# Optimization experiments

Hardware: AMD Instinct MI355X
Metric: run time of the kernel (lower is better)

## Reference

```python
import jax, jax.numpy as jnp
import numpy as np

B, K, N, M = 32, 128, 128, 256  # batch, num_classes(==n_dim), n_dim, samples-per-matrix
EPSILON = 0.1
LAMBDA_SOFTMAX = 0.1
LEARNING_RATE = 0.01
BN_EPS = 1e-5


def setup_inputs() -> dict:
    key = jax.random.key(0)
    k1, k2, k3 = jax.random.split(key, 3)
    x = jax.random.normal(k1, (B, N, M), dtype=jnp.float32)
    A = jax.random.normal(k2, (K, N, N), dtype=jnp.float32) * 0.1
    EC_proto = jnp.einsum('kij,klj->kil', A, A)  # per-class PSD prototype covariances (K,N,N)
    EC_count = jax.random.uniform(k3, (K,), dtype=jnp.float32, minval=1.0, maxval=100.0)
    return {"x": x, "EC_proto": EC_proto, "EC_count": EC_count}


def reference(x, EC_proto, EC_count):
    n = x.shape[1]
    dtype = x.dtype
    # BatchNorm1d(num_classes, affine=False, track_running_stats=False): batch stats over (N, L)
    mean = x.mean(axis=(0, 2), keepdims=True)
    var = x.var(axis=(0, 2), keepdims=True)  # biased variance, as torch uses for normalization
    x = (x - mean) / jnp.sqrt(var + BN_EPS)

    eye = jnp.eye(n, dtype=dtype)
    total = EC_count.sum()
    has_counts = total > 1e-6

    # E branch: global expansion operator
    e_alpha = jnp.where(has_counts, n / (EPSILON * EPSILON * total), jnp.zeros((), dtype))
    e = e_alpha * jnp.linalg.inv(e_alpha * EC_proto.sum(0) + eye)  # (N,N)
    e_x_z = jnp.einsum('ij,bjm->bim', e, x)  # (B,N,M)

    # C branch: per-class compression operators
    bool_depth = (EC_count != 0).astype(dtype)  # (K,)
    count_fix = EC_count + (1.0 - bool_depth)
    c_alpha = (n / (count_fix * EPSILON * EPSILON) * bool_depth)[:, None, None]  # (K,1,1)
    c = c_alpha * jnp.linalg.inv(c_alpha * EC_proto + eye[None])  # (K,N,N)
    c_x_z = jnp.einsum('kij,bjm->bkim', c, x)  # (B,K,N,M)

    # Frobenius norm per (b,k), rescaled to sum to 10 over classes
    norm = jnp.sqrt((c_x_z * c_x_z).sum(axis=(2, 3)))  # (B,K)
    norm = 10.0 * norm / norm.sum(axis=1, keepdims=True)

    pi = jax.nn.softmax(-LAMBDA_SOFTMAX * norm, axis=1) * bool_depth  # (B,K)
    gama = jnp.where(has_counts, EC_count / total, jnp.zeros_like(EC_count))  # (K,)

    z_d = e_x_z - jnp.einsum('k,bkim,bk->bim', gama, c_x_z, pi)  # (B,N,M)
    return x + LEARNING_RATE * z_d
```

## Files before the change

kernel.cpp:

```cpp
#include <hip/hip_runtime.h>
#include <math.h>

#define Bb 32
#define Kk 128
#define Nn 128
#define Mm 256
#define EPS2 0.01f
#define LAMBDA_S 0.1f
#define LR 0.01f
#define BN_EPS_C 1e-5f

#define SWZ(c) (((c) & 14) | (((c) & 1) << 4) | (((c) >> 4) & 1))

__device__ __forceinline__ float readlane_f(float v, int lane) {
  return __int_as_float(__builtin_amdgcn_readlane(__float_as_int(v), lane));
}

__global__ void kA_bn_psum(const float* __restrict__ x, const float* __restrict__ P,
                           float* __restrict__ xn, float* __restrict__ Psum) {
  int t = threadIdx.x;
  if (blockIdx.x < 128) {
    int n = blockIdx.x;
    float v[32];
    float s = 0.f, s2 = 0.f;
    #pragma unroll
    for (int b = 0; b < Bb; ++b) {
      v[b] = x[(size_t)b * (Nn * Mm) + n * Mm + t];
      s += v[b];
      s2 += v[b] * v[b];
    }
    #pragma unroll
    for (int o = 32; o > 0; o >>= 1) {
      s += __shfl_down(s, o, 64);
      s2 += __shfl_down(s2, o, 64);
    }
    __shared__ float rs[4], rs2[4];
    if ((t & 63) == 0) { rs[t >> 6] = s; rs2[t >> 6] = s2; }
    __syncthreads();
    float S = rs[0] + rs[1] + rs[2] + rs[3];
    float S2 = rs2[0] + rs2[1] + rs2[2] + rs2[3];
    float mean = S * (1.0f / (Bb * Mm));
    float var = S2 * (1.0f / (Bb * Mm)) - mean * mean;
    float rstd = 1.0f / sqrtf(var + BN_EPS_C);
    #pragma unroll
    for (int b = 0; b < Bb; ++b)
      xn[(size_t)b * (Nn * Mm) + n * Mm + t] = (v[b] - mean) * rstd;
  } else {
    int e = (blockIdx.x - 128) * 256 + t;
    float s = 0.f;
    #pragma unroll 8
    for (int k = 0; k < Kk; ++k) s += P[(size_t)k * 16384 + e];
    Psum[e] = s;
  }
}

__global__ __launch_bounds__(512, 1) void k3S(
    const float* __restrict__ P, const float* __restrict__ Psum,
    const float* __restrict__ cnt, float* __restrict__ C,
    const float* __restrict__ xn, float* __restrict__ S) {
  __shared__ __align__(16) float LB[8448];
  int bx = blockIdx.x;
  int t = threadIdx.x;

  if (bx < 129) {
    float* Mt = LB;
    float* Rb = LB + 2112;
    float* redc = LB + 4160;
    int mat = bx;
    int tx = t & 15;
    int wy = t >> 4;

    float cv = cnt[t & 127];
    float sr = cv;
    #pragma unroll
    for (int o = 32; o > 0; o >>= 1) sr += __shfl_down(sr, o, 64);
    if ((t & 63) == 0) redc[t >> 6] = sr;
    __syncthreads();
    float total = redc[0] + redc[1];
    bool has = total > 1e-6f;
    float av;
    if (mat < 128) {
      float c = cnt[mat];
      float bk = (c != 0.0f) ? 1.0f : 0.0f;
      float cfix = c + (1.0f - bk);
      av = (float)Nn / (cfix * EPS2) * bk;
    } else {
      av = has ? ((float)Nn / (EPS2 * total)) : 0.0f;
    }
    const float* src = (mat < 128) ? (P + (size_t)mat * 16384) : Psum;

    float a[4][8];
    #pragma unroll
    for (int i = 0; i < 4; ++i) {
      int row = wy * 4 + i;
      float4 p0 = *(const float4*)&src[row * 128 + tx * 8];
      float4 p1 = *(const float4*)&src[row * 128 + tx * 8 + 4];
      a[i][0] = av * p0.x; a[i][1] = av * p0.y; a[i][2] = av * p0.z; a[i][3] = av * p0.w;
      a[i][4] = av * p1.x; a[i][5] = av * p1.y; a[i][6] = av * p1.z; a[i][7] = av * p1.w;
      if (tx == (wy >> 1)) a[i][(wy & 1) * 4 + i] += 1.0f;
    }

    for (int kb = 0; kb < 8; ++kb) {
      int k0 = kb * 16;
      if ((wy >> 2) == kb) {
        int d = wy & 3;
        #pragma unroll
        for (int i = 0; i < 4; ++i) {
          *(float4*)&Rb[(d * 4 + i) * 128 + SWZ(2 * tx) * 4] =
              make_float4(a[i][0], a[i][1], a[i][2], a[i][3]);
          *(float4*)&Rb[(d * 4 + i) * 128 + SWZ(2 * tx + 1) * 4] =
              make_float4(a[i][4], a[i][5], a[i][6], a[i][7]);
        }
      }
      if ((tx >> 1) == kb) {
        int dh = tx & 1;
        #pragma unroll
        for (int i = 0; i < 4; ++i)
          #pragma unroll
          for (int j = 0; j < 8; ++j)
            Mt[(dh * 8 + j) * 132 + wy * 4 + i] = a[i][j];
      }
      __syncthreads();

      if (t < 64) {
        int l = t;
        float m[2][16];
        #pragma unroll
        for (int d = 0; d < 2; ++d)
          #pragma unroll
          for (int j = 0; j < 16; ++j)
            m[d][j] = Mt[j * 132 + 2 * l + d];
        #pragma unroll
        for (int q = 0; q < 16; ++q) {
          int lq = (k0 + q) >> 1;
          float pr[16];
          #pragma unroll
          for (int j = 0; j < 16; ++j) pr[j] = readlane_f(m[q & 1][j], lq);
          float piv = pr[q];
          float r0 = __builtin_amdgcn_rcpf(piv);
          float pinv = r0 * (2.0f - piv * r0);
          #pragma unroll
          for (int d = 0; d < 2; ++d) {
            float f = m[d][q];
            bool isp = (2 * l + d == k0 + q);
            float g = isp ? (1.0f - pinv) : f * pinv;
            #pragma unroll
            for (int j = 0; j < 16; ++j) m[d][j] = fmaf(-g, pr[j], m[d][j]);
            m[d][q] = isp ? pinv : -g;
          }
        }
        #pragma unroll
        for (int d = 0; d < 2; ++d)
          #pragma unroll
          for (int j = 0; j < 16; ++j)
            Mt[j * 132 + 2 * l + d] = m[d][j];
      }
      __syncthreads();

      if ((wy >> 2) == kb) {
        #pragma unroll
        for (int i = 0; i < 4; ++i)
          #pragma unroll
          for (int j = 0; j < 8; ++j) a[i][j] = 0.0f;
      }
      #pragma unroll
      for (int q = 0; q < 16; ++q) {
        float4 m0 = *(const float4*)&Mt[q * 132 + wy * 4];
        float4 r0 = *(const float4*)&Rb[q * 128 + SWZ(2 * tx) * 4];
        float4 r1 = *(const float4*)&Rb[q * 128 + SWZ(2 * tx + 1) * 4];
        float mq[4] = {m0.x, m0.y, m0.z, m0.w};
        float rq[8] = {r0.x, r0.y, r0.z, r0.w, r1.x, r1.y, r1.z, r1.w};
        #pragma unroll
        for (int i = 0; i < 4; ++i)
          #pragma unroll
          for (int j = 0; j < 8; ++j)
            a[i][j] = fmaf(mq[i], rq[j], a[i][j]);
      }
      if ((tx >> 1) == kb) {
        int dh = tx & 1;
        #pragma unroll
        for (int j = 0; j < 8; ++j) {
          float4 v0 = *(const float4*)&Mt[(dh * 8 + j) * 132 + wy * 4];
          a[0][j] = v0.x; a[1][j] = v0.y; a[2][j] = v0.z; a[3][j] = v0.w;
        }
      }
      __syncthreads();
    }

    float* dst = C + (size_t)mat * 16384;
    #pragma unroll
    for (int i = 0; i < 4; ++i) {
      int row = wy * 4 + i;
      float4 v0 = make_float4(av * a[i][0], av * a[i][1], av * a[i][2], av * a[i][3]);
      float4 v1 = make_float4(av * a[i][4], av * a[i][5], av * a[i][6], av * a[i][7]);
      *(float4*)&dst[row * 128 + tx * 8] = v0;
      *(float4*)&dst[row * 128 + tx * 8 + 4] = v1;
    }
  } else {
    int bxx = bx - 129;
    int b = bxx >> 1;
    int jbase = (bxx & 1) * 64;
    float* X = LB;
    int tx = t & 15, wy = t >> 4;
    float acc[4][4] = {};
    for (int mc = 0; mc < Mm; mc += 64) {
      __syncthreads();
      #pragma unroll
      for (int c = 0; c < 16; ++c) {
        int e = c * 512 + t;
        int i = e >> 6, mm = e & 63;
        X[i * 65 + mm] = xn[(size_t)b * (Nn * Mm) + i * Mm + mc + mm];
      }
      __syncthreads();
      for (int mm = 0; mm < 64; ++mm) {
        float ai[4], bj[4];
        #pragma unroll
        for (int q = 0; q < 4; ++q) ai[q] = X[(wy * 4 + q) * 65 + mm];
        #pragma unroll
        for (int q = 0; q < 4; ++q) bj[q] = X[(jbase + tx * 4 + q) * 65 + mm];
        #pragma unroll
        for (int qi = 0; qi < 4; ++qi)
          #pragma unroll
          for (int qj = 0; qj < 4; ++qj)
            acc[qi][qj] = fmaf(ai[qi], bj[qj], acc[qi][qj]);
      }
    }
    float* dst = S + (size_t)b * 16384;
    #pragma unroll
    for (int qi = 0; qi < 4; ++qi) {
      float4 v = make_float4(acc[qi][0], acc[qi][1], acc[qi][2], acc[qi][3]);
      *(float4*)&dst[(wy * 4 + qi) * 128 + jbase + tx * 4] = v;
    }
  }
}

__global__ __launch_bounds__(256, 1) void kGN(const float* __restrict__ C,
                                              const float* __restrict__ S,
                                              float* __restrict__ norm2h) {
  __shared__ __align__(16) float LB[128 * 128];
  __shared__ float redb[4][32];
  int k = blockIdx.x >> 2, qh = blockIdx.x & 3;
  int t = threadIdx.x;
  const float* src = C + (size_t)k * 16384;
  for (int c = 0; c < 64; ++c) LB[c * 256 + t] = src[c * 256 + t];
  __syncthreads();
  int tx = t & 15, ty = t >> 4;
  int i0 = ty * 8, j0 = qh * 32 + tx * 2;
  float acc[8][2] = {};
  #pragma unroll 2
  for (int l = 0; l < 128; ++l) {
    float ai[8];
    *(float4*)&ai[0] = *(const float4*)&LB[l * 128 + i0];
    *(float4*)&ai[4] = *(const float4*)&LB[l * 128 + i0 + 4];
    float2 bj = *(const float2*)&LB[l * 128 + j0];
    #pragma unroll
    for (int qi = 0; qi < 8; ++qi) {
      acc[qi][0] = fmaf(ai[qi], bj.x, acc[qi][0]);
      acc[qi][1] = fmaf(ai[qi], bj.y, acc[qi][1]);
    }
  }
  __syncthreads();
  #pragma unroll
  for (int qi = 0; qi < 8; ++qi)
    *(float2*)&LB[(i0 + qi) * 32 + tx * 2] = make_float2(acc[qi][0], acc[qi][1]);
  __syncthreads();
  float nacc[32];
  #pragma unroll
  for (int b = 0; b < 32; ++b) nacc[b] = 0.0f;
  #pragma unroll
  for (int q = 0; q < 4; ++q) {
    int el = (q * 256 + t) * 4;
    float4 g = *(const float4*)&LB[el];
    int i = el >> 5, jl = el & 31;
    const float* sb = S + i * 128 + qh * 32 + jl;
    #pragma unroll
    for (int b = 0; b < 32; ++b) {
      float4 sv = *(const float4*)&sb[(size_t)b * 16384];
      nacc[b] = fmaf(g.x, sv.x, nacc[b]);
      nacc[b] = fmaf(g.y, sv.y, nacc[b]);
      nacc[b] = fmaf(g.z, sv.z, nacc[b]);
      nacc[b] = fmaf(g.w, sv.w, nacc[b]);
    }
  }
  #pragma unroll
  for (int b = 0; b < 32; ++b) {
    float v = nacc[b];
    #pragma unroll
    for (int o = 32; o > 0; o >>= 1) v += __shfl_down(v, o, 64);
    nacc[b] = v;
  }
  if ((t & 63) == 0) {
    int w = t >> 6;
    #pragma unroll
    for (int b = 0; b < 32; ++b) redb[w][b] = nacc[b];
  }
  __syncthreads();
  if (t < 32)
    norm2h[(size_t)k * 128 + qh * 32 + t] =
        redb[0][t] + redb[1][t] + redb[2][t] + redb[3][t];
}

__global__ void k7n(const float* __restrict__ norm2h, const float* __restrict__ cnt,
                    float* __restrict__ wT) {
  int b = blockIdx.x;
  int k = threadIdx.x;
  const float* nh = norm2h + (size_t)k * 128 + b;
  float n2 = nh[0] + nh[32] + nh[64] + nh[96];
  float norm = sqrtf(fmaxf(n2, 0.0f));
  float cv = cnt[k];
  __shared__ float r1[2], r2[2], r3[2];
  float tt = cv, r = norm;
  #pragma unroll
  for (int o = 32; o > 0; o >>= 1) {
    tt += __shfl_down(tt, o, 64);
    r += __shfl_down(r, o, 64);
  }
  if ((k & 63) == 0) { r1[k >> 6] = tt; r2[k >> 6] = r; }
  __syncthreads();
  float total = r1[0] + r1[1];
  float sumn = r2[0] + r2[1];
  float nr = 10.0f * norm / fmaxf(sumn, 1e-30f);
  float ex = expf(-LAMBDA_S * nr);
  float e2 = ex;
  #pragma unroll
  for (int o = 32; o > 0; o >>= 1) e2 += __shfl_down(e2, o, 64);
  if ((k & 63) == 0) r3[k >> 6] = e2;
  __syncthreads();
  float sume = r3[0] + r3[1];
  float bk = (cv != 0.0f) ? 1.0f : 0.0f;
  float pi = (ex / sume) * bk;
  float gama = (total > 1e-6f) ? (cv / total) : 0.0f;
  wT[k * 32 + b] = gama * pi;
}

__global__ __launch_bounds__(256, 1) void k8_k(const float* __restrict__ C,
                                               const float* __restrict__ E,
                                               const float* __restrict__ wT,
                                               float* __restrict__ F) {
  int e = blockIdx.x * 256 + threadIdx.x;
  int b0 = blockIdx.y * 8;
  float acc[8];
  float ev = E[e];
  #pragma unroll
  for (int b = 0; b < 8; ++b) acc[b] = ev;
  #pragma unroll 4
  for (int k = 0; k < 128; ++k) {
    float cv = C[(size_t)k * 16384 + e];
    const float* wk = wT + k * 32 + b0;
    #pragma unroll
    for (int b = 0; b < 8; ++b) acc[b] = fmaf(-wk[b], cv, acc[b]);
  }
  #pragma unroll
  for (int b = 0; b < 8; ++b) F[(size_t)(b0 + b) * 16384 + e] = acc[b];
}

__global__ __launch_bounds__(256, 1) void k9_k(const float* __restrict__ F,
                                               const float* __restrict__ xn,
                                               float* __restrict__ out) {
  int bx = blockIdx.x;
  int b = bx >> 3, y = bx & 7;
  int mq = y >> 1, ih = y & 1;
  __shared__ __align__(16) float Ft[64 * 68];
  __shared__ __align__(16) float Xt[64 * 68];
  int t = threadIdx.x;
  int tx = t & 15, ty = t >> 4;
  float acc[4][4] = {};
  for (int jc = 0; jc < 128; jc += 64) {
    __syncthreads();
    #pragma unroll
    for (int q = 0; q < 4; ++q) {
      int e = q * 256 + t;
      int i = e >> 4, j4 = e & 15;
      *(float4*)&Ft[i * 68 + j4 * 4] =
          *(const float4*)&F[(size_t)b * 16384 + (ih * 64 + i) * 128 + jc + j4 * 4];
    }
    #pragma unroll
    for (int q = 0; q < 4; ++q) {
      int e = q * 256 + t;
      int jj = e >> 4, m4 = e & 15;
      *(float4*)&Xt[jj * 68 + m4 * 4] =
          *(const float4*)&xn[(size_t)b * (Nn * Mm) + (jc + jj) * Mm + mq * 64 + m4 * 4];
    }
    __syncthreads();
    for (int j4 = 0; j4 < 16; ++j4) {
      float4 fi[4], xm[4];
      #pragma unroll
      for (int r = 0; r < 4; ++r)
        fi[r] = *(const float4*)&Ft[(ty * 4 + r) * 68 + j4 * 4];
      #pragma unroll
      for (int r = 0; r < 4; ++r)
        xm[r] = *(const float4*)&Xt[(j4 * 4 + r) * 68 + tx * 4];
      #pragma unroll
      for (int qi = 0; qi < 4; ++qi) {
        #pragma unroll
        for (int qm = 0; qm < 4; ++qm) {
          float xv = ((const float*)&xm[0])[qm];
          acc[qi][qm] = fmaf(fi[qi].x, xv, acc[qi][qm]);
          xv = ((const float*)&xm[1])[qm];
          acc[qi][qm] = fmaf(fi[qi].y, xv, acc[qi][qm]);
          xv = ((const float*)&xm[2])[qm];
          acc[qi][qm] = fmaf(fi[qi].z, xv, acc[qi][qm]);
          xv = ((const float*)&xm[3])[qm];
          acc[qi][qm] = fmaf(fi[qi].w, xv, acc[qi][qm]);
        }
      }
    }
  }
  int i0 = ih * 64 + ty * 4, m0 = mq * 64 + tx * 4;
  #pragma unroll
  for (int qi = 0; qi < 4; ++qi) {
    float4 xv = *(const float4*)&xn[(size_t)b * (Nn * Mm) + (i0 + qi) * Mm + m0];
    float4 o;
    o.x = fmaf(LR, acc[qi][0], xv.x);
    o.y = fmaf(LR, acc[qi][1], xv.y);
    o.z = fmaf(LR, acc[qi][2], xv.z);
    o.w = fmaf(LR, acc[qi][3], xv.w);
    *(float4*)&out[(size_t)b * (Nn * Mm) + (i0 + qi) * Mm + m0] = o;
  }
}

extern "C" void kernel_launch(void* const* d_in, const int* in_sizes, int n_in,
                              void* d_out, int out_size, void* d_ws, size_t ws_size,
                              hipStream_t stream) {
  const float* x = (const float*)d_in[0];
  const float* P = (const float*)d_in[1];
  const float* cnt = (const float*)d_in[2];
  float* out = (float*)d_out;

  float* ws = (float*)d_ws;
  float* xn = ws;
  float* C = xn + 1048576;
  float* S = C + 2113536;
  float* norm2h = S + 524288;
  float* wT = norm2h + 16384;
  float* F = wT + 4096;
  float* Psum = F + 524288;
  size_t need_bytes = (size_t)((Psum + 16384) - ws) * sizeof(float);
  if (ws_size < need_bytes) return;

  hipLaunchKernelGGL(kA_bn_psum, dim3(192), dim3(256), 0, stream, x, P, xn, Psum);
  hipLaunchKernelGGL(k3S, dim3(193), dim3(512), 0, stream, P, Psum, cnt, C, xn, S);
  hipLaunchKernelGGL(kGN, dim3(512), dim3(256), 0, stream, C, S, norm2h);
  hipLaunchKernelGGL(k7n, dim3(32), dim3(128), 0, stream, norm2h, cnt, wT);
  hipLaunchKernelGGL(k8_k, dim3(64, 4), dim3(256), 0, stream, C,
                     C + (size_t)128 * 16384, wT, F);
  hipLaunchKernelGGL(k9_k, dim3(256), dim3(256), 0, stream, F, xn, out);
}
```

Measured before the change: 160.0 us.

## Defer batchnorm into raw Gram and k9 load, drop normalized x buffer

```diff
diff --git a/kernel.cpp b/kernel.cpp
--- a/kernel.cpp
+++ b/kernel.cpp
@@ -16,48 +16,20 @@
   return __int_as_float(__builtin_amdgcn_readlane(__float_as_int(v), lane));
 }
 
-__global__ void kA_bn_psum(const float* __restrict__ x, const float* __restrict__ P,
-                           float* __restrict__ xn, float* __restrict__ Psum) {
-  int t = threadIdx.x;
-  if (blockIdx.x < 128) {
-    int n = blockIdx.x;
-    float v[32];
-    float s = 0.f, s2 = 0.f;
-    #pragma unroll
-    for (int b = 0; b < Bb; ++b) {
-      v[b] = x[(size_t)b * (Nn * Mm) + n * Mm + t];
-      s += v[b];
-      s2 += v[b] * v[b];
-    }
-    #pragma unroll
-    for (int o = 32; o > 0; o >>= 1) {
-      s += __shfl_down(s, o, 64);
-      s2 += __shfl_down(s2, o, 64);
-    }
-    __shared__ float rs[4], rs2[4];
-    if ((t & 63) == 0) { rs[t >> 6] = s; rs2[t >> 6] = s2; }
-    __syncthreads();
-    float S = rs[0] + rs[1] + rs[2] + rs[3];
-    float S2 = rs2[0] + rs2[1] + rs2[2] + rs2[3];
-    float mean = S * (1.0f / (Bb * Mm));
-    float var = S2 * (1.0f / (Bb * Mm)) - mean * mean;
-    float rstd = 1.0f / sqrtf(var + BN_EPS_C);
-    #pragma unroll
-    for (int b = 0; b < Bb; ++b)
-      xn[(size_t)b * (Nn * Mm) + n * Mm + t] = (v[b] - mean) * rstd;
-  } else {
-    int e = (blockIdx.x - 128) * 256 + t;
-    float s = 0.f;
-    #pragma unroll 8
-    for (int k = 0; k < Kk; ++k) s += P[(size_t)k * 16384 + e];
-    Psum[e] = s;
-  }
-}
-
-__global__ __launch_bounds__(512, 1) void k3S(
+__global__ void kPre(const float* __restrict__ P, float* __restrict__ Psum) {
+  int e = blockIdx.x * 256 + threadIdx.x;
+  float s = 0.f;
+  #pragma unroll 8
+  for (int k = 0; k < Kk; ++k) s += P[(size_t)k * 16384 + e];
+  Psum[e] = s;
+}
+
+__global__ __launch_bounds__(512, 1) void kIR(
     const float* __restrict__ P, const float* __restrict__ Psum,
     const float* __restrict__ cnt, float* __restrict__ C,
-    const float* __restrict__ xn, float* __restrict__ S) {
+    const float* __restrict__ x, float* __restrict__ R,
+    float* __restrict__ rbuf, float* __restrict__ meanB,
+    float* __restrict__ rstdB) {
   __shared__ __align__(16) float LB[8448];
   int bx = blockIdx.x;
   int t = threadIdx.x;
@@ -196,22 +168,27 @@
       *(float4*)&dst[row * 128 + tx * 8] = v0;
       *(float4*)&dst[row * 128 + tx * 8 + 4] = v1;
     }
-  } else {
+  } else if (bx < 193) {
     int bxx = bx - 129;
     int b = bxx >> 1;
     int jbase = (bxx & 1) * 64;
     float* X = LB;
     int tx = t & 15, wy = t >> 4;
     float acc[4][4] = {};
+    float rsum = 0.f;
     for (int mc = 0; mc < Mm; mc += 64) {
       __syncthreads();
       #pragma unroll
       for (int c = 0; c < 16; ++c) {
         int e = c * 512 + t;
         int i = e >> 6, mm = e & 63;
-        X[i * 65 + mm] = xn[(size_t)b * (Nn * Mm) + i * Mm + mc + mm];
+        X[i * 65 + mm] = x[(size_t)b * (Nn * Mm) + i * Mm + mc + mm];
       }
       __syncthreads();
+      if (t < 128) {
+        #pragma unroll
+        for (int mm = 0; mm < 64; ++mm) rsum += X[t * 65 + mm];
+      }
       for (int mm = 0; mm < 64; ++mm) {
         float ai[4], bj[4];
         #pragma unroll
@@ -225,22 +202,53 @@
             acc[qi][qj] = fmaf(ai[qi], bj[qj], acc[qi][qj]);
       }
     }
-    float* dst = S + (size_t)b * 16384;
+    float* dst = R + (size_t)b * 16384;
     #pragma unroll
     for (int qi = 0; qi < 4; ++qi) {
       float4 v = make_float4(acc[qi][0], acc[qi][1], acc[qi][2], acc[qi][3]);
       *(float4*)&dst[(wy * 4 + qi) * 128 + jbase + tx * 4] = v;
     }
+    if (jbase == 0 && t < 128) rbuf[b * 128 + t] = rsum;
+  } else {
+    int n = bx - 193;
+    int m = t & 255, bh = t >> 8;
+    float s = 0.f, s2 = 0.f;
+    #pragma unroll
+    for (int q = 0; q < 16; ++q) {
+      float v = x[(size_t)(bh * 16 + q) * (Nn * Mm) + n * Mm + m];
+      s += v; s2 += v * v;
+    }
+    #pragma unroll
+    for (int o = 32; o > 0; o >>= 1) {
+      s += __shfl_down(s, o, 64);
+      s2 += __shfl_down(s2, o, 64);
+    }
+    if ((t & 63) == 0) { LB[t >> 6] = s; LB[16 + (t >> 6)] = s2; }
+    __syncthreads();
+    if (t == 0) {
+      float S = 0.f, S2 = 0.f;
+      #pragma unroll
+      for (int w = 0; w < 8; ++w) { S += LB[w]; S2 += LB[16 + w]; }
+      float mean = S * (1.0f / (Bb * Mm));
+      float var = S2 * (1.0f / (Bb * Mm)) - mean * mean;
+      meanB[n] = mean;
+      rstdB[n] = 1.0f / sqrtf(var + BN_EPS_C);
+    }
   }
 }
 
 __global__ __launch_bounds__(256, 1) void kGN(const float* __restrict__ C,
-                                              const float* __restrict__ S,
+                                              const float* __restrict__ R,
+                                              const float* __restrict__ rbuf,
+                                              const float* __restrict__ meanB,
+                                              const float* __restrict__ rstdB,
                                               float* __restrict__ norm2h) {
   __shared__ __align__(16) float LB[128 * 128];
   __shared__ float redb[4][32];
+  __shared__ float muL[128], rsL[128], uL[128];
   int k = blockIdx.x >> 2, qh = blockIdx.x & 3;
   int t = threadIdx.x;
+  if (t < 128) { muL[t] = meanB[t]; rsL[t] = rstdB[t]; }
   const float* src = C + (size_t)k * 16384;
   for (int c = 0; c < 64; ++c) LB[c * 256 + t] = src[c * 256 + t];
   __syncthreads();
@@ -260,10 +268,21 @@
     }
   }
   __syncthreads();
-  #pragma unroll
-  for (int qi = 0; qi < 8; ++qi)
-    *(float2*)&LB[(i0 + qi) * 32 + tx * 2] = make_float2(acc[qi][0], acc[qi][1]);
-  __syncthreads();
+  float sj0 = rsL[j0], sj1 = rsL[j0 + 1];
+  #pragma unroll
+  for (int qi = 0; qi < 8; ++qi) {
+    float si = rsL[i0 + qi];
+    *(float2*)&LB[(i0 + qi) * 32 + tx * 2] =
+        make_float2(acc[qi][0] * si * sj0, acc[qi][1] * si * sj1);
+  }
+  __syncthreads();
+  if (t < 128) {
+    float u = 0.f;
+    #pragma unroll
+    for (int jl = 0; jl < 32; ++jl)
+      u = fmaf(LB[t * 32 + jl], muL[qh * 32 + jl], u);
+    uL[t] = u;
+  }
   float nacc[32];
   #pragma unroll
   for (int b = 0; b < 32; ++b) nacc[b] = 0.0f;
@@ -272,7 +291,7 @@
     int el = (q * 256 + t) * 4;
     float4 g = *(const float4*)&LB[el];
     int i = el >> 5, jl = el & 31;
-    const float* sb = S + i * 128 + qh * 32 + jl;
+    const float* sb = R + i * 128 + qh * 32 + jl;
     #pragma unroll
     for (int b = 0; b < 32; ++b) {
       float4 sv = *(const float4*)&sb[(size_t)b * 16384];
@@ -295,9 +314,13 @@
     for (int b = 0; b < 32; ++b) redb[w][b] = nacc[b];
   }
   __syncthreads();
-  if (t < 32)
+  if (t < 32) {
+    float corr = 0.f;
+    for (int i = 0; i < 128; ++i)
+      corr = fmaf(uL[i], 256.0f * muL[i] - 2.0f * rbuf[t * 128 + i], corr);
     norm2h[(size_t)k * 128 + qh * 32 + t] =
-        redb[0][t] + redb[1][t] + redb[2][t] + redb[3][t];
+        redb[0][t] + redb[1][t] + redb[2][t] + redb[3][t] + corr;
+  }
 }
 
 __global__ void k7n(const float* __restrict__ norm2h, const float* __restrict__ cnt,
@@ -355,14 +378,18 @@
 }
 
 __global__ __launch_bounds__(256, 1) void k9_k(const float* __restrict__ F,
-                                               const float* __restrict__ xn,
+                                               const float* __restrict__ x,
+                                               const float* __restrict__ meanB,
+                                               const float* __restrict__ rstdB,
                                                float* __restrict__ out) {
   int bx = blockIdx.x;
   int b = bx >> 3, y = bx & 7;
   int mq = y >> 1, ih = y & 1;
   __shared__ __align__(16) float Ft[64 * 68];
   __shared__ __align__(16) float Xt[64 * 68];
+  __shared__ float muL[128], rsL[128];
   int t = threadIdx.x;
+  if (t < 128) { muL[t] = meanB[t]; rsL[t] = rstdB[t]; }
   int tx = t & 15, ty = t >> 4;
   float acc[4][4] = {};
   for (int jc = 0; jc < 128; jc += 64) {
@@ -378,8 +405,10 @@
     for (int q = 0; q < 4; ++q) {
       int e = q * 256 + t;
       int jj = e >> 4, m4 = e & 15;
+      float4 g = *(const float4*)&x[(size_t)b * (Nn * Mm) + (jc + jj) * Mm + mq * 64 + m4 * 4];
+      float mu = muL[jc + jj], rs = rsL[jc + jj];
       *(float4*)&Xt[jj * 68 + m4 * 4] =
-          *(const float4*)&xn[(size_t)b * (Nn * Mm) + (jc + jj) * Mm + mq * 64 + m4 * 4];
+          make_float4((g.x - mu) * rs, (g.y - mu) * rs, (g.z - mu) * rs, (g.w - mu) * rs);
     }
     __syncthreads();
     for (int j4 = 0; j4 < 16; ++j4) {
@@ -409,12 +438,13 @@
   int i0 = ih * 64 + ty * 4, m0 = mq * 64 + tx * 4;
   #pragma unroll
   for (int qi = 0; qi < 4; ++qi) {
-    float4 xv = *(const float4*)&xn[(size_t)b * (Nn * Mm) + (i0 + qi) * Mm + m0];
+    float4 xv = *(const float4*)&x[(size_t)b * (Nn * Mm) + (i0 + qi) * Mm + m0];
+    float mu = muL[i0 + qi], rs = rsL[i0 + qi];
     float4 o;
-    o.x = fmaf(LR, acc[qi][0], xv.x);
-    o.y = fmaf(LR, acc[qi][1], xv.y);
-    o.z = fmaf(LR, acc[qi][2], xv.z);
-    o.w = fmaf(LR, acc[qi][3], xv.w);
+    o.x = fmaf(LR, acc[qi][0], (xv.x - mu) * rs);
+    o.y = fmaf(LR, acc[qi][1], (xv.y - mu) * rs);
+    o.z = fmaf(LR, acc[qi][2], (xv.z - mu) * rs);
+    o.w = fmaf(LR, acc[qi][3], (xv.w - mu) * rs);
     *(float4*)&out[(size_t)b * (Nn * Mm) + (i0 + qi) * Mm + m0] = o;
   }
 }
@@ -428,21 +458,25 @@
   float* out = (float*)d_out;
 
   float* ws = (float*)d_ws;
-  float* xn = ws;
-  float* C = xn + 1048576;
-  float* S = C + 2113536;
-  float* norm2h = S + 524288;
+  float* C = ws;
+  float* R = C + 2113536;
+  float* norm2h = R + 524288;
   float* wT = norm2h + 16384;
   float* F = wT + 4096;
   float* Psum = F + 524288;
-  size_t need_bytes = (size_t)((Psum + 16384) - ws) * sizeof(float);
+  float* rbuf = Psum + 16384;
+  float* meanB = rbuf + 4096;
+  float* rstdB = meanB + 128;
+  size_t need_bytes = (size_t)((rstdB + 128) - ws) * sizeof(float);
   if (ws_size < need_bytes) return;
 
-  hipLaunchKernelGGL(kA_bn_psum, dim3(192), dim3(256), 0, stream, x, P, xn, Psum);
-  hipLaunchKernelGGL(k3S, dim3(193), dim3(512), 0, stream, P, Psum, cnt, C, xn, S);
-  hipLaunchKernelGGL(kGN, dim3(512), dim3(256), 0, stream, C, S, norm2h);
+  hipLaunchKernelGGL(kPre, dim3(64), dim3(256), 0, stream, P, Psum);
+  hipLaunchKernelGGL(kIR, dim3(321), dim3(512), 0, stream, P, Psum, cnt, C, x, R,
+                     rbuf, meanB, rstdB);
+  hipLaunchKernelGGL(kGN, dim3(512), dim3(256), 0, stream, C, R, rbuf, meanB,
+                     rstdB, norm2h);
   hipLaunchKernelGGL(k7n, dim3(32), dim3(128), 0, stream, norm2h, cnt, wT);
   hipLaunchKernelGGL(k8_k, dim3(64, 4), dim3(256), 0, stream, C,
                      C + (size_t)128 * 16384, wT, F);
-  hipLaunchKernelGGL(k9_k, dim3(256), dim3(256), 0, stream, F, xn, out);
-}
+  hipLaunchKernelGGL(k9_k, dim3(256), dim3(256), 0, stream, F, x, meanB, rstdB, out);
+}
```

After: 162.5 us. About the same (+1.6%).
